# Optimization experiments

Hardware: AMD Instinct MI355X
Metric: run time of the kernel (lower is better)

## Reference

```python
import jax, jax.numpy as jnp
import numpy as np

B, M, T, L, K = 64, 16, 2048, 64, 32
N = T - L + 1  # 1985 sliding-window positions


def setup_inputs() -> dict:
    key = jax.random.key(0)
    k1, k2, k3 = jax.random.split(key, 3)
    x = jax.random.normal(k1, (B, M, T), dtype=jnp.float32)
    # shapelets initialized uniform(-1, 1) as in nn.init.uniform_
    shapelets = jax.random.uniform(k2, (K, L), dtype=jnp.float32, minval=-1.0, maxval=1.0)
    # penalty maps (learned; zeros at init, random here for a non-trivial weighting)
    penalty_maps = 0.1 * jax.random.normal(k3, (K, M, N), dtype=jnp.float32)
    return {"x": x, "shapelets": shapelets, "penalty_maps": penalty_maps}


def reference(x, shapelets, penalty_maps):
    # x: (B, M, T); shapelets: (K, L); penalty_maps: (K, M, N)
    Lw = shapelets.shape[1]
    n_pos = x.shape[2] - Lw + 1
    # sliding-window view: (B, M, N, L), equivalent to torch unfold(dim=2, size=L, step=1)
    idx = jnp.arange(n_pos)[:, None] + jnp.arange(Lw)[None, :]
    sub = x[:, :, idx]  # (B, M, N, L)

    def per_shapelet(args):
        shp, pmap = args  # (L,), (M, N)
        # raw squared L2 distance over window, per channel/position: (B, M, N)
        raw = jnp.sum((sub - shp[None, None, None, :]) ** 2, axis=3)
        pen = jax.nn.elu(-pmap) + 2.0  # (M, N)
        wd = jnp.sum(raw * pen[None], axis=1)  # sum over channels -> (B, N)
        return jnp.min(wd, axis=1)  # min over positions -> (B,)

    # sequential map over the K shapelets avoids a Kx blow-up of the (B,M,N,L) intermediate
    feats = jax.lax.map(per_shapelet, (shapelets, penalty_maps))  # (K, B)
    return feats.T  # (B, K)
```

## Files before the change

kernel.cpp:

```cpp
#include <hip/hip_runtime.h>
#include <hip/hip_bf16.h>

#define B_ 64
#define M_ 16
#define T_ 2048
#define L_ 64
#define K_ 32
#define N_ (T_ - L_ + 1)
#define NQP 512
#define XBS 2112
#define SQS 2048
#define TN 64
#define NTH 256
#define XRW 80
#define SQWP 20

typedef __attribute__((ext_vector_type(8))) short bf16x8;
typedef __attribute__((ext_vector_type(4))) float f32x4;

__device__ __forceinline__ unsigned short f2bf(float f) {
    __hip_bfloat16 h = __float2bfloat16(f);
    return __builtin_bit_cast(unsigned short, h);
}
__device__ __forceinline__ unsigned fun16(unsigned lo, unsigned hi) {
    return (unsigned)(((((unsigned long long)hi) << 32) | lo) >> 16);
}

__global__ void pen_init_kernel(const float* __restrict__ pmap,
                                const float* __restrict__ shp,
                                float* __restrict__ pen_t,
                                float* __restrict__ ss_ws,
                                unsigned* __restrict__ out) {
    const int gid = blockIdx.x * 256 + threadIdx.x;
    if (gid < B_ * K_) out[gid] = 0x7F800000u;
    if (gid < K_) {
        float s = 0.f;
        for (int l = 0; l < L_; ++l) { float v = shp[gid * L_ + l]; s = fmaf(v, v, s); }
        ss_ws[gid] = s;
    }
    if (gid < M_ * NQP * K_) {
        const int m  = gid >> 14;
        const int rem = gid & 16383;
        const int nq = rem >> 5;
        const int k  = rem & 31;
        const float* src = pmap + ((size_t)k * M_ + m) * N_;
        float4 r; float* pr = (float*)&r;
#pragma unroll
        for (int i = 0; i < 4; ++i) {
            int n = 4 * nq + i; if (n >= N_) n = N_ - 1;
            const float p = src[n];
            pr[i] = (p < 0.f) ? (2.f - p) : (__expf(-p) + 1.f);
        }
        *(float4*)(pen_t + (size_t)gid * 4) = r;
    }
}

__global__ __launch_bounds__(256)
void xprep_kernel(const float* __restrict__ x,
                  unsigned short* __restrict__ xbf,
                  float* __restrict__ sqwin) {
    __shared__ __align__(16) float xrow[T_ + 64];
    const int r = blockIdx.x;
    const int tid = threadIdx.x;
    const float* src = x + (size_t)r * T_;
#pragma unroll
    for (int i = 0; i < 2; ++i) {
        const int i4 = 4 * (tid + 256 * i);
        float4 v = *(const float4*)(src + i4);
        *(float4*)&xrow[i4] = v;
        ushort4 sv = { f2bf(v.x), f2bf(v.y), f2bf(v.z), f2bf(v.w) };
        *(ushort4*)(xbf + (size_t)r * XBS + i4) = sv;
    }
    if (tid < 16) *(float4*)&xrow[T_ + 4 * tid] = make_float4(0.f, 0.f, 0.f, 0.f);
    if (tid < 16) {
        ushort4 z = { 0, 0, 0, 0 };
        *(ushort4*)(xbf + (size_t)r * XBS + T_ + 4 * tid) = z;
    }
    __syncthreads();
    const int n0t = 8 * tid;
    float s = 0.f;
#pragma unroll
    for (int qd = 0; qd < 16; ++qd) {
        float4 v = *(const float4*)&xrow[n0t + 4 * qd];
        s = fmaf(v.x, v.x, s); s = fmaf(v.y, v.y, s);
        s = fmaf(v.z, v.z, s); s = fmaf(v.w, v.w, s);
    }
    float* dst = sqwin + (size_t)r * SQS + n0t;
    dst[0] = s;
#pragma unroll
    for (int d = 1; d < 8; ++d) {
        float a = xrow[n0t + d + L_ - 1], rm = xrow[n0t + d - 1];
        s += a * a - rm * rm;
        dst[d] = s;
    }
}

__global__ __launch_bounds__(NTH, 3)
void shapelet_mfma_kernel(const unsigned short* __restrict__ xbf,
                          const float* __restrict__ sqwin,
                          const float* __restrict__ shp,
                          const float* __restrict__ pen_t,
                          const float* __restrict__ ss_ws,
                          unsigned* __restrict__ out) {
    __shared__ __align__(16) unsigned short xw[4][M_][4][XRW];
    __shared__ __align__(16) float sqw[4][M_][SQWP];

    const int tid = threadIdx.x;
    const int lane = tid & 63;
    const int w  = tid >> 6;
    const int rl = lane & 15;
    const int q  = lane >> 4;
    const int n0 = blockIdx.x * TN;
    const int b  = blockIdx.y;
    const int nb = n0 + 16 * w;

    for (int i = lane; i < M_ * 19; i += 64) {
        const int m = i / 19, j4 = (i - m * 19) * 4;
        const unsigned short* s8 = xbf + ((size_t)(b * M_ + m)) * XBS + nb + j4;
        uint2 a = *(const uint2*)s8;
        uint2 c = *(const uint2*)(s8 + 4);
        const unsigned u0 = a.x, u1 = a.y, u2 = c.x, u3 = c.y;
        const unsigned a01 = fun16(u0, u1);
        const unsigned a12 = fun16(u1, u2);
        const unsigned a23 = fun16(u2, u3);
        uint2 p;
        p.x = u0;  p.y = u1;  *(uint2*)&xw[w][m][0][j4] = p;
        p.x = a01; p.y = a12; *(uint2*)&xw[w][m][1][j4] = p;
        p.x = u1;  p.y = u2;  *(uint2*)&xw[w][m][2][j4] = p;
        p.x = a12; p.y = a23; *(uint2*)&xw[w][m][3][j4] = p;
    }
    {
        const int m = lane >> 2, n4 = (lane & 3) * 4;
        float4 v = *(const float4*)(sqwin + ((size_t)(b * M_ + m)) * SQS + nb + n4);
        *(float4*)&sqw[w][m][n4] = v;
    }
    bf16x8 bfr[2][2];
#pragma unroll
    for (int t = 0; t < 2; ++t)
#pragma unroll
        for (int h = 0; h < 2; ++h) {
            const float* sp_ = shp + (16 * t + rl) * L_ + 8 * q + 32 * h;
            float4 v0 = *(const float4*)sp_;
            float4 v1 = *(const float4*)(sp_ + 4);
            union { unsigned short us[8]; bf16x8 v; } cv;
            cv.us[0] = f2bf(v0.x); cv.us[1] = f2bf(v0.y);
            cv.us[2] = f2bf(v0.z); cv.us[3] = f2bf(v0.w);
            cv.us[4] = f2bf(v1.x); cv.us[5] = f2bf(v1.y);
            cv.us[6] = f2bf(v1.z); cv.us[7] = f2bf(v1.w);
            bfr[t][h] = cv.v;
        }

    const float ssk0 = ss_ws[rl], ssk1 = ss_ws[16 + rl];
    const int sp = rl & 3;
    const int e0s = 8 * q + (rl & ~3);
    const int eqi = e0s >> 2;
    const int nrow = nb + 4 * q;

    const int nq_l = (n0 >> 2) + 4 * w + q;
    const float* pt0 = pen_t + (((size_t)nq_l) * K_ + rl) * 4;

    f32x4 wd0 = (f32x4)0.f, wd1 = (f32x4)0.f;
    const f32x4 zero = (f32x4)0.f;

#pragma unroll 2
    for (int m = 0; m < M_; ++m) {
        float4 p0 = *(const float4*)(pt0 + (size_t)m * (NQP * K_ * 4));
        float4 p1 = *(const float4*)(pt0 + (size_t)m * (NQP * K_ * 4) + 64);

        const uint2* prow = (const uint2*)&xw[w][m][sp][0];
        uint2 lo0 = prow[eqi],     hi0 = prow[eqi + 1];
        uint2 lo1 = prow[eqi + 8], hi1 = prow[eqi + 9];
        union { uint2 u2[2]; bf16x8 v; } fa0, fa1;
        fa0.u2[0] = lo0; fa0.u2[1] = hi0;
        fa1.u2[0] = lo1; fa1.u2[1] = hi1;

        f32x4 c0_ = __builtin_amdgcn_mfma_f32_16x16x32_bf16(fa0.v, bfr[0][0], zero, 0, 0, 0);
        c0_       = __builtin_amdgcn_mfma_f32_16x16x32_bf16(fa1.v, bfr[0][1], c0_, 0, 0, 0);
        f32x4 c1_ = __builtin_amdgcn_mfma_f32_16x16x32_bf16(fa0.v, bfr[1][0], zero, 0, 0, 0);
        c1_       = __builtin_amdgcn_mfma_f32_16x16x32_bf16(fa1.v, bfr[1][1], c1_, 0, 0, 0);

        f32x4 sq = *(const f32x4*)&sqw[w][m][4 * q];
        const float pe0[4] = { p0.x, p0.y, p0.z, p0.w };
        const float pe1[4] = { p1.x, p1.y, p1.z, p1.w };
#pragma unroll
        for (int r = 0; r < 4; ++r) {
            float t0v = fmaf(-2.f, c0_[r], sq[r] + ssk0);
            wd0[r] = fmaf(pe0[r], t0v, wd0[r]);
            float t1v = fmaf(-2.f, c1_[r], sq[r] + ssk1);
            wd1[r] = fmaf(pe1[r], t1v, wd1[r]);
        }
    }

#pragma unroll
    for (int t = 0; t < 2; ++t) {
        float lmin = __int_as_float(0x7F800000);
        const f32x4& wdv = t ? wd1 : wd0;
#pragma unroll
        for (int r = 0; r < 4; ++r) {
            if (nrow + r < N_) lmin = fminf(lmin, wdv[r]);
        }
        lmin = fminf(lmin, __shfl_xor(lmin, 16));
        lmin = fminf(lmin, __shfl_xor(lmin, 32));
        if (q == 0) {
            atomicMin(out + (size_t)b * K_ + 16 * t + rl,
                      __float_as_uint(fmaxf(lmin, 0.f)));
        }
    }
}

extern "C" void kernel_launch(void* const* d_in, const int* in_sizes, int n_in,
                              void* d_out, int out_size, void* d_ws, size_t ws_size,
                              hipStream_t stream) {
    const float* x    = (const float*)d_in[0];
    const float* shp  = (const float*)d_in[1];
    const float* pmap = (const float*)d_in[2];
    unsigned* out = (unsigned*)d_out;

    float* pen_t = (float*)d_ws;
    float* ss_ws = pen_t + (size_t)M_ * NQP * K_ * 4;
    unsigned short* xbf = (unsigned short*)(ss_ws + 64);
    float* sqwin = (float*)(xbf + (size_t)B_ * M_ * XBS);

    pen_init_kernel<<<dim3(M_ * NQP * K_ / 256), dim3(256), 0, stream>>>(
        pmap, shp, pen_t, ss_ws, out);
    xprep_kernel<<<dim3(B_ * M_), dim3(256), 0, stream>>>(x, xbf, sqwin);

    dim3 grid((N_ + TN - 1) / TN, B_);
    shapelet_mfma_kernel<<<grid, dim3(NTH), 0, stream>>>(
        xbf, sqwin, shp, pen_t, ss_ws, out);
}
```

Before: 102.1 us.

## Store penalty weights as fp16, prefetch them into registers, pre-convert shapelets to bf16

The penalty map workspace is now written as fp16 instead of fp32, which halves the bytes the main kernel reads for weights. All 16 channels' penalty values are loaded into registers at kernel start, before the LDS staging, so their global-load latency overlaps the setup work. The shapelets are also converted to bf16 once in the init kernel instead of in every block, and the channel loop is fully unrolled. The risks are higher register pressure under launch bounds of 3 blocks per SIMD and a small precision loss in the penalty weights.

```diff
diff --git a/kernel.cpp b/kernel.cpp
--- a/kernel.cpp
+++ b/kernel.cpp
@@ -1,4 +1,5 @@
 #include <hip/hip_runtime.h>
+#include <hip/hip_fp16.h>
 #include <hip/hip_bf16.h>
 
 #define B_ 64
@@ -22,14 +23,18 @@
     __hip_bfloat16 h = __float2bfloat16(f);
     return __builtin_bit_cast(unsigned short, h);
 }
+__device__ __forceinline__ float h2f(unsigned short u) {
+    return __half2float(__builtin_bit_cast(__half, u));
+}
 __device__ __forceinline__ unsigned fun16(unsigned lo, unsigned hi) {
     return (unsigned)(((((unsigned long long)hi) << 32) | lo) >> 16);
 }
 
 __global__ void pen_init_kernel(const float* __restrict__ pmap,
                                 const float* __restrict__ shp,
-                                float* __restrict__ pen_t,
+                                unsigned short* __restrict__ pen_h,
                                 float* __restrict__ ss_ws,
+                                unsigned short* __restrict__ shp_bf,
                                 unsigned* __restrict__ out) {
     const int gid = blockIdx.x * 256 + threadIdx.x;
     if (gid < B_ * K_) out[gid] = 0x7F800000u;
@@ -38,20 +43,26 @@
         for (int l = 0; l < L_; ++l) { float v = shp[gid * L_ + l]; s = fmaf(v, v, s); }
         ss_ws[gid] = s;
     }
+    if (gid < K_ * 16) {
+        float4 v = *(const float4*)(shp + gid * 4);
+        ushort4 sv = { f2bf(v.x), f2bf(v.y), f2bf(v.z), f2bf(v.w) };
+        *(ushort4*)(shp_bf + gid * 4) = sv;
+    }
     if (gid < M_ * NQP * K_) {
         const int m  = gid >> 14;
         const int rem = gid & 16383;
         const int nq = rem >> 5;
         const int k  = rem & 31;
         const float* src = pmap + ((size_t)k * M_ + m) * N_;
-        float4 r; float* pr = (float*)&r;
+        ushort4 o; unsigned short* po = (unsigned short*)&o;
 #pragma unroll
         for (int i = 0; i < 4; ++i) {
             int n = 4 * nq + i; if (n >= N_) n = N_ - 1;
             const float p = src[n];
-            pr[i] = (p < 0.f) ? (2.f - p) : (__expf(-p) + 1.f);
-        }
-        *(float4*)(pen_t + (size_t)gid * 4) = r;
+            const float pe = (p < 0.f) ? (2.f - p) : (__expf(-p) + 1.f);
+            po[i] = __builtin_bit_cast(unsigned short, __float2half(pe));
+        }
+        *(ushort4*)(pen_h + (size_t)gid * 4) = o;
     }
 }
 
@@ -98,8 +109,8 @@
 __global__ __launch_bounds__(NTH, 3)
 void shapelet_mfma_kernel(const unsigned short* __restrict__ xbf,
                           const float* __restrict__ sqwin,
-                          const float* __restrict__ shp,
-                          const float* __restrict__ pen_t,
+                          const unsigned short* __restrict__ shp_bf,
+                          const unsigned short* __restrict__ pen_h,
                           const float* __restrict__ ss_ws,
                           unsigned* __restrict__ out) {
     __shared__ __align__(16) unsigned short xw[4][M_][4][XRW];
@@ -113,6 +124,15 @@
     const int n0 = blockIdx.x * TN;
     const int b  = blockIdx.y;
     const int nb = n0 + 16 * w;
+
+    const int nq_l = (n0 >> 2) + 4 * w + q;
+    const unsigned short* pb = pen_h + (((size_t)nq_l) * K_ + rl) * 4;
+    ushort4 penr0[M_], penr1[M_];
+#pragma unroll
+    for (int m = 0; m < M_; ++m) {
+        penr0[m] = *(const ushort4*)(pb + (size_t)m * (NQP * K_ * 4));
+        penr1[m] = *(const ushort4*)(pb + (size_t)m * (NQP * K_ * 4) + 64);
+    }
 
     for (int i = lane; i < M_ * 19; i += 64) {
         const int m = i / 19, j4 = (i - m * 19) * 4;
@@ -139,15 +159,9 @@
     for (int t = 0; t < 2; ++t)
 #pragma unroll
         for (int h = 0; h < 2; ++h) {
-            const float* sp_ = shp + (16 * t + rl) * L_ + 8 * q + 32 * h;
-            float4 v0 = *(const float4*)sp_;
-            float4 v1 = *(const float4*)(sp_ + 4);
-            union { unsigned short us[8]; bf16x8 v; } cv;
-            cv.us[0] = f2bf(v0.x); cv.us[1] = f2bf(v0.y);
-            cv.us[2] = f2bf(v0.z); cv.us[3] = f2bf(v0.w);
-            cv.us[4] = f2bf(v1.x); cv.us[5] = f2bf(v1.y);
-            cv.us[6] = f2bf(v1.z); cv.us[7] = f2bf(v1.w);
-            bfr[t][h] = cv.v;
+            uint4 v = *(const uint4*)(shp_bf + (16 * t + rl) * L_ + 8 * q + 32 * h);
+            union { uint4 u; bf16x8 b; } cv; cv.u = v;
+            bfr[t][h] = cv.b;
         }
 
     const float ssk0 = ss_ws[rl], ssk1 = ss_ws[16 + rl];
@@ -156,17 +170,11 @@
     const int eqi = e0s >> 2;
     const int nrow = nb + 4 * q;
 
-    const int nq_l = (n0 >> 2) + 4 * w + q;
-    const float* pt0 = pen_t + (((size_t)nq_l) * K_ + rl) * 4;
-
     f32x4 wd0 = (f32x4)0.f, wd1 = (f32x4)0.f;
     const f32x4 zero = (f32x4)0.f;
 
-#pragma unroll 2
+#pragma unroll
     for (int m = 0; m < M_; ++m) {
-        float4 p0 = *(const float4*)(pt0 + (size_t)m * (NQP * K_ * 4));
-        float4 p1 = *(const float4*)(pt0 + (size_t)m * (NQP * K_ * 4) + 64);
-
         const uint2* prow = (const uint2*)&xw[w][m][sp][0];
         uint2 lo0 = prow[eqi],     hi0 = prow[eqi + 1];
         uint2 lo1 = prow[eqi + 8], hi1 = prow[eqi + 9];
@@ -180,8 +188,10 @@
         c1_       = __builtin_amdgcn_mfma_f32_16x16x32_bf16(fa1.v, bfr[1][1], c1_, 0, 0, 0);
 
         f32x4 sq = *(const f32x4*)&sqw[w][m][4 * q];
-        const float pe0[4] = { p0.x, p0.y, p0.z, p0.w };
-        const float pe1[4] = { p1.x, p1.y, p1.z, p1.w };
+        const float pe0[4] = { h2f(penr0[m].x), h2f(penr0[m].y),
+                               h2f(penr0[m].z), h2f(penr0[m].w) };
+        const float pe1[4] = { h2f(penr1[m].x), h2f(penr1[m].y),
+                               h2f(penr1[m].z), h2f(penr1[m].w) };
 #pragma unroll
         for (int r = 0; r < 4; ++r) {
             float t0v = fmaf(-2.f, c0_[r], sq[r] + ssk0);
@@ -216,16 +226,17 @@
     const float* pmap = (const float*)d_in[2];
     unsigned* out = (unsigned*)d_out;
 
-    float* pen_t = (float*)d_ws;
-    float* ss_ws = pen_t + (size_t)M_ * NQP * K_ * 4;
-    unsigned short* xbf = (unsigned short*)(ss_ws + 64);
+    unsigned short* pen_h = (unsigned short*)d_ws;
+    float* ss_ws = (float*)(pen_h + (size_t)M_ * NQP * K_ * 4);
+    unsigned short* shp_bf = (unsigned short*)(ss_ws + 64);
+    unsigned short* xbf = shp_bf + K_ * L_;
     float* sqwin = (float*)(xbf + (size_t)B_ * M_ * XBS);
 
     pen_init_kernel<<<dim3(M_ * NQP * K_ / 256), dim3(256), 0, stream>>>(
-        pmap, shp, pen_t, ss_ws, out);
+        pmap, shp, pen_h, ss_ws, shp_bf, out);
     xprep_kernel<<<dim3(B_ * M_), dim3(256), 0, stream>>>(x, xbf, sqwin);
 
     dim3 grid((N_ + TN - 1) / TN, B_);
     shapelet_mfma_kernel<<<grid, dim3(NTH), 0, stream>>>(
-        xbf, sqwin, shp, pen_t, ss_ws, out);
-}
+        xbf, sqwin, shp_bf, pen_h, ss_ws, out);
+}
```

Measured after the change: 116.0 us. 1.14x slower.
